# Optimization experiments

Measured on AMD Instinct MI355X. Metric: run time of the kernel, lower is better.

## Reference

```python
import jax, jax.numpy as jnp
import numpy as np
import math

LUT_RES = 512
TWO_PI = 2.0 * math.pi
# LUT tables: sin/cos sampled uniformly over [0, 2*pi)
_SIN_TABLE = jnp.sin(jnp.arange(LUT_RES, dtype=jnp.float32) * (TWO_PI / LUT_RES))


def _lut_idx(phase):
    # phase mod 2*pi mapped to [0, LUT_RES) integer bin (floor lookup)
    frac = jnp.mod(phase, TWO_PI) * (1.0 / TWO_PI)
    return (frac * LUT_RES).astype(jnp.int32) % LUT_RES


def setup_inputs() -> dict:
    key = jax.random.key(0)
    k1, k2, k3 = jax.random.split(key, 3)
    B, S, E, N = 2, 1024, 128, 512
    x = jax.random.normal(k1, (B, S, E), dtype=jnp.float32)
    w = jax.random.normal(k2, (E, N), dtype=jnp.float32) * 0.1          # init_freq_scale
    b = jax.random.uniform(k3, (E, N), dtype=jnp.float32) * TWO_PI      # init_offset_scale
    t = jnp.arange(S, dtype=jnp.float32)
    return {"x": x, "w": w, "b": b, "t": t}


def reference(x, w, b, t):
    # phase: (B, S, E, N) = w*x (broadcast outer product) + b + t
    phase = (w[None, None, :, :] * x[:, :, :, None]
             + b[None, None, :, :]
             + t[None, :, None, None])
    sin_vals = _SIN_TABLE[_lut_idx(phase)]   # LUT sin lookup
    return sin_vals.sum(axis=2)              # reduce over embed_dim -> (B, S, N)
```

## Files before the change

kernel.cpp:

```cpp
#include <hip/hip_runtime.h>
#include <math.h>


constexpr int E_DIM = 128;
constexpr int N_DIM = 512;
constexpr int ST    = 8;
constexpr int TPB   = 256;
constexpr int EC    = 4;
constexpr int ECH   = E_DIM / EC;

__global__ __launch_bounds__(TPB) void sin_layer_partial(
    const float* __restrict__ x,
    const float* __restrict__ w,
    const float* __restrict__ bv_,
    const float* __restrict__ t,
    float* __restrict__ part,
    int S, int BS)
{
    constexpr float SCALE  = 512.0f * 0.15915493667125702f;
    constexpr float INV512 = 1.0f / 512.0f;

    const int bid = blockIdx.x;
    const int ec  = bid & (EC - 1);
    const int nh  = (bid >> 2) & 1;
    const int g   = bid >> 3;
    const int n   = nh * TPB + threadIdx.x;
    const int bs0 = g * ST;
    const int e0  = ec * ECH;

    float tn[ST];
    float acc[ST];
    const float* xr[ST];
#pragma unroll
    for (int i = 0; i < ST; ++i) {
        const int bs = bs0 + i;
        const int s  = (bs >= S) ? (bs - S) : bs;
        tn[i]  = t[s] * SCALE;
        xr[i]  = x + (size_t)bs * E_DIM + e0;
        acc[i] = 0.0f;
    }

    const float* wp = w   + (size_t)e0 * N_DIM + n;
    const float* bp = bv_ + (size_t)e0 * N_DIM + n;

#pragma unroll 4
    for (int e = 0; e < ECH; ++e) {
        const float wv = wp[(size_t)e * N_DIM];
        const float bb = bp[(size_t)e * N_DIM];
        const float wn = wv * SCALE;
        float btn[ST];
#pragma unroll
        for (int i = 0; i < ST; ++i)
            btn[i] = __fmaf_rn(bb, SCALE, tn[i]);
#pragma unroll
        for (int i = 0; i < ST; ++i) {
            const float xv = xr[i][e];
            float u = __fmaf_rn(wn, xv, btn[i]);
            float k = floorf(u);
            acc[i] += __builtin_amdgcn_sinf(k * INV512);
        }
    }

    float* pp = part + (size_t)ec * BS * N_DIM;
#pragma unroll
    for (int i = 0; i < ST; ++i) {
        pp[(size_t)(bs0 + i) * N_DIM + n] = acc[i];
    }
}

__global__ __launch_bounds__(TPB) void sin_layer_reduce(
    const float* __restrict__ part,
    float* __restrict__ out,
    int nvec)
{
    const int i = blockIdx.x * TPB + threadIdx.x;
    if (i >= nvec) return;
    const float4* p = (const float4*)part;
    float4 a = p[i];
    float4 b = p[i + (size_t)nvec];
    float4 c = p[i + (size_t)2 * nvec];
    float4 d = p[i + (size_t)3 * nvec];
    float4 o;
    o.x = (a.x + b.x) + (c.x + d.x);
    o.y = (a.y + b.y) + (c.y + d.y);
    o.z = (a.z + b.z) + (c.z + d.z);
    o.w = (a.w + b.w) + (c.w + d.w);
    ((float4*)out)[i] = o;
}

extern "C" void kernel_launch(void* const* d_in, const int* in_sizes, int n_in,
                              void* d_out, int out_size, void* d_ws, size_t ws_size,
                              hipStream_t stream) {
    const float* x = (const float*)d_in[0];
    const float* w = (const float*)d_in[1];
    const float* b = (const float*)d_in[2];
    const float* t = (const float*)d_in[3];
    float* out  = (float*)d_out;
    float* part = (float*)d_ws;

    const int S  = in_sizes[3];
    const int BS = in_sizes[0] / E_DIM;

    const int grid1 = (BS / ST) * 2 * EC;
    sin_layer_partial<<<grid1, TPB, 0, stream>>>(x, w, b, t, part, S, BS);

    const int nvec  = out_size / 4;
    const int grid2 = (nvec + TPB - 1) / TPB;
    sin_layer_reduce<<<grid2, TPB, 0, stream>>>(part, out, nvec);
}
```

Baseline: 92.35 us.

## Replace hardware sin with bank-replicated shared-memory LUT and larger blocks

Replaces the per-element hardware sin with a lookup into a shared-memory sine table. The table is replicated 32 times and interleaved so each lane reads its own bank copy, which avoids bank conflicts. The phase is scaled by 65536/2π so the floored integer carries both the bin index and room for the lane offset. Blocks grow to 1024 threads, covering all 512 columns and 16 rows, which cuts the number of blocks. This trades transcendental throughput for LDS bandwidth, at the cost of 64KB of shared memory per block plus a table fill in every block, and it lowers occupancy.

```diff
diff --git a/kernel.cpp b/kernel.cpp
--- a/kernel.cpp
+++ b/kernel.cpp
@@ -4,10 +4,12 @@
 
 constexpr int E_DIM = 128;
 constexpr int N_DIM = 512;
-constexpr int ST    = 8;
-constexpr int TPB   = 256;
 constexpr int EC    = 4;
 constexpr int ECH   = E_DIM / EC;
+constexpr int RB    = 16;
+constexpr int RT    = 8;
+constexpr int TPB   = 1024;
+constexpr int NCPY  = 32;
 
 __global__ __launch_bounds__(TPB) void sin_layer_partial(
     const float* __restrict__ x,
@@ -17,25 +19,39 @@
     float* __restrict__ part,
     int S, int BS)
 {
-    constexpr float SCALE  = 512.0f * 0.15915493667125702f;
-    constexpr float INV512 = 1.0f / 512.0f;
+    constexpr float SCALE128 = 65536.0f * 0.15915493667125702f;
+    constexpr float INV512   = 1.0f / 512.0f;
+
+    __shared__ float lut32[512 * NCPY];
+
+    {
+        const int tid = threadIdx.x;
+#pragma unroll
+        for (int k = 0; k < (512 * NCPY) / TPB; ++k) {
+            const int j = tid + k * TPB;
+            lut32[j] = __builtin_amdgcn_sinf((float)(j >> 5) * INV512);
+        }
+    }
+    __syncthreads();
 
     const int bid = blockIdx.x;
     const int ec  = bid & (EC - 1);
-    const int nh  = (bid >> 2) & 1;
-    const int g   = bid >> 3;
-    const int n   = nh * TPB + threadIdx.x;
-    const int bs0 = g * ST;
+    const int rg  = bid >> 2;
+    const int tid = threadIdx.x;
+    const int n   = tid & (N_DIM - 1);
+    const int rh  = tid >> 9;
+    const int bs0 = rg * RB + rh * RT;
     const int e0  = ec * ECH;
+    const int co4 = (tid & 31) << 2;
 
-    float tn[ST];
-    float acc[ST];
-    const float* xr[ST];
+    float tn[RT];
+    float acc[RT];
+    const float* xr[RT];
 #pragma unroll
-    for (int i = 0; i < ST; ++i) {
+    for (int i = 0; i < RT; ++i) {
         const int bs = bs0 + i;
         const int s  = (bs >= S) ? (bs - S) : bs;
-        tn[i]  = t[s] * SCALE;
+        tn[i]  = t[s] * SCALE128;
         xr[i]  = x + (size_t)bs * E_DIM + e0;
         acc[i] = 0.0f;
     }
@@ -45,35 +61,34 @@
 
 #pragma unroll 4
     for (int e = 0; e < ECH; ++e) {
-        const float wv = wp[(size_t)e * N_DIM];
+        const float wn = wp[(size_t)e * N_DIM] * SCALE128;
         const float bb = bp[(size_t)e * N_DIM];
-        const float wn = wv * SCALE;
-        float btn[ST];
+        float btn[RT];
 #pragma unroll
-        for (int i = 0; i < ST; ++i)
-            btn[i] = __fmaf_rn(bb, SCALE, tn[i]);
+        for (int i = 0; i < RT; ++i)
+            btn[i] = __fmaf_rn(bb, SCALE128, tn[i]);
 #pragma unroll
-        for (int i = 0; i < ST; ++i) {
+        for (int i = 0; i < RT; ++i) {
             const float xv = xr[i][e];
-            float u = __fmaf_rn(wn, xv, btn[i]);
-            float k = floorf(u);
-            acc[i] += __builtin_amdgcn_sinf(k * INV512);
+            const float u  = __fmaf_rn(wn, xv, btn[i]);
+            const int   iu = (int)floorf(u);
+            const int  idx = ((iu & 65408) | co4) >> 2;
+            acc[i] += lut32[idx];
         }
     }
 
     float* pp = part + (size_t)ec * BS * N_DIM;
 #pragma unroll
-    for (int i = 0; i < ST; ++i) {
+    for (int i = 0; i < RT; ++i)
         pp[(size_t)(bs0 + i) * N_DIM + n] = acc[i];
-    }
 }
 
-__global__ __launch_bounds__(TPB) void sin_layer_reduce(
+__global__ __launch_bounds__(256) void sin_layer_reduce(
     const float* __restrict__ part,
     float* __restrict__ out,
     int nvec)
 {
-    const int i = blockIdx.x * TPB + threadIdx.x;
+    const int i = blockIdx.x * 256 + threadIdx.x;
     if (i >= nvec) return;
     const float4* p = (const float4*)part;
     float4 a = p[i];
@@ -101,10 +116,10 @@
     const int S  = in_sizes[3];
     const int BS = in_sizes[0] / E_DIM;
 
-    const int grid1 = (BS / ST) * 2 * EC;
+    const int grid1 = (BS / RB) * EC;
     sin_layer_partial<<<grid1, TPB, 0, stream>>>(x, w, b, t, part, S, BS);
 
     const int nvec  = out_size / 4;
-    const int grid2 = (nvec + TPB - 1) / TPB;
-    sin_layer_reduce<<<grid2, TPB, 0, stream>>>(part, out, nvec);
+    const int grid2 = (nvec + 255) / 256;
+    sin_layer_reduce<<<grid2, 256, 0, stream>>>(part, out, nvec);
 }
```

New measurement: 96.24 us. 4.2% more time.
